# Kernel tuning notes

Hardware: AMD Instinct MI355X
Metric: run time of the kernel (lower is better)

The kernel has to match this reference:

```python
import jax, jax.numpy as jnp
import numpy as np

B, T, I, H = 256, 2000, 23, 128


def setup_inputs() -> dict:
    key = jax.random.key(0)
    ks = jax.random.split(key, 5)
    s = 1.0 / np.sqrt(H)  # PyTorch GRU init bound
    return {
        "x": jax.random.normal(ks[0], (B, T, I), dtype=jnp.float32),
        "W_ih": jax.random.uniform(ks[1], (3 * H, I), jnp.float32, -s, s),
        "W_hh": jax.random.uniform(ks[2], (3 * H, H), jnp.float32, -s, s),
        "b_ih": jax.random.uniform(ks[3], (3 * H,), jnp.float32, -s, s),
        "b_hh": jax.random.uniform(ks[4], (3 * H,), jnp.float32, -s, s),
    }


def reference(x, W_ih, W_hh, b_ih, b_hh):
    """Single-layer unidirectional GRU (PyTorch gate order r,z,n),
    followed by mean over time. Dropout is identity (eval mode)."""
    Bb, Tt, _ = x.shape
    Hh = W_hh.shape[1]
    # Precompute input-side gate projections for all timesteps: [T, B, 3H]
    gx = jnp.einsum('bti,gi->tbg', x, W_ih) + b_ih

    def step(h, g):
        gh = h @ W_hh.T + b_hh                               # [B, 3H]
        r = jax.nn.sigmoid(g[:, :Hh] + gh[:, :Hh])
        z = jax.nn.sigmoid(g[:, Hh:2 * Hh] + gh[:, Hh:2 * Hh])
        n = jnp.tanh(g[:, 2 * Hh:] + r * gh[:, 2 * Hh:])
        h_new = (1.0 - z) * n + z * h
        return h_new, h_new

    h0 = jnp.zeros((Bb, Hh), dtype=x.dtype)
    _, hs = jax.lax.scan(step, h0, gx)                       # hs: [T, B, H]
    return jnp.mean(hs, axis=0)                              # [B, H]
```

## Files before the change

### kernel.cpp

```cpp
#include <hip/hip_runtime.h>


#define Bb 256
#define Tt 2000
#define Ii 23
#define Hh 128

typedef float v2f __attribute__((ext_vector_type(2)));
typedef float v4f __attribute__((ext_vector_type(4)));

template <int N> struct ic { static constexpr int v = N; };

template <int ctrl>
__device__ __forceinline__ float dpp_movf(float v) {
    int r = __builtin_amdgcn_update_dpp(0, __builtin_bit_cast(int, v),
                                        ctrl, 0xf, 0xf, true);
    return __builtin_bit_cast(float, r);
}
__device__ __forceinline__ float swz_xor4(float v) {
    int r = __builtin_amdgcn_ds_swizzle(__builtin_bit_cast(int, v), 0x101F);
    return __builtin_bit_cast(float, r);
}
__device__ __forceinline__ void pk_fma(v2f& a, v2f b, v2f c) {
    asm("v_pk_fma_f32 %0, %1, %2, %0" : "+v"(a) : "v"(b), "v"(c));
}
__device__ __forceinline__ v2f pk_mul(v2f b, v2f c) {
    v2f d;
    asm("v_pk_mul_f32 %0, %1, %2" : "=v"(d) : "v"(b), "v"(c));
    return d;
}
__device__ __forceinline__ float fexp2(float x) {
#if __has_builtin(__builtin_amdgcn_exp2f)
    return __builtin_amdgcn_exp2f(x);
#else
    return exp2f(x);
#endif
}
__device__ __forceinline__ void bar_lds() {
    asm volatile("s_waitcnt lgkmcnt(0)\n\ts_barrier" ::: "memory");
}

__device__ __forceinline__ float fold16x8(const float a[8]) {
    float b0 = a[0] + dpp_movf<0xB1>(a[4]);
    float b1 = a[1] + dpp_movf<0xB1>(a[5]);
    float b2 = a[2] + dpp_movf<0xB1>(a[6]);
    float b3 = a[3] + dpp_movf<0xB1>(a[7]);
    float c0 = b0 + dpp_movf<0x4E>(b2);
    float c1 = b1 + dpp_movf<0x4E>(b3);
    float d  = c0 + swz_xor4(c1);
    return d + dpp_movf<0x128>(d);
}
__device__ __forceinline__ float fold16x4(const float a[4]) {
    float b0 = a[0] + dpp_movf<0xB1>(a[0]);
    float b1 = a[1] + dpp_movf<0xB1>(a[1]);
    float b2 = a[2] + dpp_movf<0xB1>(a[2]);
    float b3 = a[3] + dpp_movf<0xB1>(a[3]);
    float c0 = b0 + dpp_movf<0x4E>(b2);
    float c1 = b1 + dpp_movf<0x4E>(b3);
    float d  = c0 + swz_xor4(c1);
    return d + dpp_movf<0x128>(d);
}

__global__ __launch_bounds__(512, 2)
void gru_fused(const float* __restrict__ x,
               const float* __restrict__ W_ih,
               const float* __restrict__ W_hh,
               const float* __restrict__ b_ih,
               const float* __restrict__ b_hh,
               float* __restrict__ out)
{
    const int b   = blockIdx.x;
    const int tid = threadIdx.x;
    const int wid = tid >> 6;
    const int l   = tid & 63;
    const int kt  = l & 15;
    const int kb  = kt * 8;
    const int p   = ((kt & 1) << 2) | (kt & 2) | ((kt >> 2) & 1);
    const int p2  = (kt & 2) | ((kt >> 2) & 1);
    const int jbase = wid * 16 + ((l >> 4) << 2);

    __shared__ __align__(16) float h_db[2][16][12];

    const float L2E = 1.4426950408889634f;
    const float K2  = 2.0f * L2E;

    v2f wrz2[8][4];
    #pragma unroll
    for (int i = 0; i < 8; ++i) {
        const int u = i ^ p;
        const int g = (u >> 2) * Hh + jbase + (u & 3);
        const v2f* wp = reinterpret_cast<const v2f*>(W_hh + (size_t)g * Hh + kb);
        #pragma unroll
        for (int kk = 0; kk < 4; ++kk) {
            v2f w = wp[kk];
            w[0] *= L2E; w[1] *= L2E;
            wrz2[i][kk] = w;
        }
    }
    v2f wn2[4][4];
    #pragma unroll
    for (int q = 0; q < 4; ++q) {
        const int g = 2 * Hh + jbase + (q ^ p2);
        const v2f* wp = reinterpret_cast<const v2f*>(W_hh + (size_t)g * Hh + kb);
        #pragma unroll
        for (int kk = 0; kk < 4; ++kk) {
            v2f w = wp[kk];
            w[0] *= K2; w[1] *= K2;
            wn2[q][kk] = w;
        }
    }

    const int xi0  = (kt < 7) ? kt * 2 : 7 + kt;
    const int xoff = (kt < 7) ? 1 : 0;
    v2f wx2[8];
    #pragma unroll
    for (int i = 0; i < 8; ++i) {
        const int u = i ^ p;
        const int g = (u >> 2) * Hh + jbase + (u & 3);
        wx2[i][0] = W_ih[(size_t)g * Ii + xi0] * L2E;
        wx2[i][1] = xoff ? W_ih[(size_t)g * Ii + xi0 + 1] * L2E : 0.0f;
    }
    v2f wxn2[4];
    #pragma unroll
    for (int q = 0; q < 4; ++q) {
        const int g = 2 * Hh + jbase + (q ^ p2);
        wxn2[q][0] = W_ih[(size_t)g * Ii + xi0] * K2;
        wxn2[q][1] = xoff ? W_ih[(size_t)g * Ii + xi0 + 1] * K2 : 0.0f;
    }

    const int gp = (p >> 2) * Hh + jbase + (p & 3);
    const float brz_l = (b_ih[gp] + b_hh[gp]) * L2E;
    const int jn = jbase + p2;
    const float bhn_l = b_hh[2 * Hh + jn] * K2;
    const float bxn_l = b_ih[2 * Hh + jn] * K2;

    const float* xrow = x + (size_t)b * Tt * Ii;

    if (tid < Hh) h_db[0][tid >> 3][tid & 7] = 0.0f;
    float x0a = xrow[xi0],      x0b = xrow[xi0 + xoff];
    float x1a = xrow[Ii + xi0], x1b = xrow[Ii + xi0 + xoff];
    int xob = 2 * Ii + xi0;
    float h_reg = 0.0f, acc_mean = 0.0f;
    const bool writer = ((kt & 9) == 0);
    const int  jw = jbase + p;
    bar_lds();

    auto body = [&](auto CUR, int s) {
        constexpr int cur = decltype(CUR)::v;
        const int step = s + cur;

        const v4f hA = *reinterpret_cast<const v4f*>(&h_db[cur][kt][0]);
        const v4f hB = *reinterpret_cast<const v4f*>(&h_db[cur][kt][4]);
        v2f hp[4];
        hp[0] = __builtin_shufflevector(hA, hA, 0, 1);
        hp[1] = __builtin_shufflevector(hA, hA, 2, 3);
        hp[2] = __builtin_shufflevector(hB, hB, 0, 1);
        hp[3] = __builtin_shufflevector(hB, hB, 2, 3);

        v2f acc[8], accn[4];
        #pragma unroll
        for (int i = 0; i < 8; ++i) acc[i] = pk_mul(wrz2[i][0], hp[0]);
        #pragma unroll
        for (int q = 0; q < 4; ++q) accn[q] = pk_mul(wn2[q][0], hp[0]);
        #pragma unroll
        for (int kk = 1; kk < 4; ++kk) {
            #pragma unroll
            for (int i = 0; i < 8; ++i) pk_fma(acc[i], wrz2[i][kk], hp[kk]);
            #pragma unroll
            for (int q = 0; q < 4; ++q) pk_fma(accn[q], wn2[q][kk], hp[kk]);
        }

        v2f xpv;
        if constexpr (cur == 0) { xpv[0] = x0a; xpv[1] = x0b; }
        else                    { xpv[0] = x1a; xpv[1] = x1b; }
        #pragma unroll
        for (int i = 0; i < 8; ++i) pk_fma(acc[i], wx2[i], xpv);
        float arz[8];
        #pragma unroll
        for (int i = 0; i < 8; ++i) arz[i] = acc[i][0] + acc[i][1];
        float an[4], axn[4];
        #pragma unroll
        for (int q = 0; q < 4; ++q) {
            an[q] = accn[q][0] + accn[q][1];
            v2f tq = pk_mul(wxn2[q], xpv);
            axn[q] = tq[0] + tq[1];
        }

        if constexpr (cur == 0) { x0a = xrow[xob]; x0b = xrow[xob + xoff]; }
        else                    { x1a = xrow[xob]; x1b = xrow[xob + xoff]; }
        if (step + 3 < Tt) xob += Ii;

        const float rz_tot = fold16x8(arz) + brz_l;
        const float ghn = fold16x4(an) + bhn_l;
        const float gxn = fold16x4(axn) + bxn_l;

        const float zin = dpp_movf<0xB1>(rz_tot);
        const float r  = __builtin_amdgcn_rcpf(1.0f + fexp2(-rz_tot));
        const float z  = __builtin_amdgcn_rcpf(1.0f + fexp2(-zin));
        const float npre = fmaf(r, ghn, gxn);
        const float tt2  = __builtin_amdgcn_rcpf(1.0f + fexp2(-npre));
        const float nn   = fmaf(2.0f, tt2, -1.0f);
        const float h_new = fmaf(z, h_reg - nn, nn);
        h_reg = h_new;
        if (writer) {
            acc_mean += h_new;
            h_db[cur ^ 1][jw >> 3][jw & 7] = h_new;
        }
        bar_lds();
    };

    for (int s = 0; s < Tt; s += 2) {
        body(ic<0>{}, s);
        body(ic<1>{}, s);
    }

    if (writer) out[(size_t)b * Hh + jw] = acc_mean * (1.0f / Tt);
}

extern "C" void kernel_launch(void* const* d_in, const int* in_sizes, int n_in,
                              void* d_out, int out_size, void* d_ws, size_t ws_size,
                              hipStream_t stream) {
    const float* x    = (const float*)d_in[0];
    const float* W_ih = (const float*)d_in[1];
    const float* W_hh = (const float*)d_in[2];
    const float* b_ih = (const float*)d_in[3];
    const float* b_hh = (const float*)d_in[4];
    float* out = (float*)d_out;

    gru_fused<<<Bb, 512, 0, stream>>>(x, W_ih, W_hh, b_ih, b_hh, out);
}
```

Before: 1.275 ms.

## Repartition GRU recurrence: 4 lanes per hidden unit with 32-wide K slices

Changes the per-step work split so that each hidden unit j is computed by 4 adjacent lanes, each holding 32 K-elements of the r, z and n weight rows, replacing the 16-lane split with permuted gate assignment. The cross-lane reduction shrinks to two DPP adds per gate and the ds_swizzle step is gone, which shortens the serial critical path of each timestep. In exchange every lane now evaluates all three gates, so the transcendental work is duplicated across the 4 lanes. The h broadcast layout in LDS changes to 4 rows of 36 floats, and each lane now reads eight 16-byte vectors per step.

```diff
diff --git a/kernel.cpp b/kernel.cpp
--- a/kernel.cpp
+++ b/kernel.cpp
@@ -15,10 +15,6 @@
 __device__ __forceinline__ float dpp_movf(float v) {
     int r = __builtin_amdgcn_update_dpp(0, __builtin_bit_cast(int, v),
                                         ctrl, 0xf, 0xf, true);
-    return __builtin_bit_cast(float, r);
-}
-__device__ __forceinline__ float swz_xor4(float v) {
-    int r = __builtin_amdgcn_ds_swizzle(__builtin_bit_cast(int, v), 0x101F);
     return __builtin_bit_cast(float, r);
 }
 __device__ __forceinline__ void pk_fma(v2f& a, v2f b, v2f c) {
@@ -36,29 +32,15 @@
     return exp2f(x);
 #endif
 }
+__device__ __forceinline__ v2f pinv(v2f v) { asm("" : "+v"(v)); return v; }
+__device__ __forceinline__ float pinf(float v) { asm("" : "+v"(v)); return v; }
 __device__ __forceinline__ void bar_lds() {
     asm volatile("s_waitcnt lgkmcnt(0)\n\ts_barrier" ::: "memory");
 }
-
-__device__ __forceinline__ float fold16x8(const float a[8]) {
-    float b0 = a[0] + dpp_movf<0xB1>(a[4]);
-    float b1 = a[1] + dpp_movf<0xB1>(a[5]);
-    float b2 = a[2] + dpp_movf<0xB1>(a[6]);
-    float b3 = a[3] + dpp_movf<0xB1>(a[7]);
-    float c0 = b0 + dpp_movf<0x4E>(b2);
-    float c1 = b1 + dpp_movf<0x4E>(b3);
-    float d  = c0 + swz_xor4(c1);
-    return d + dpp_movf<0x128>(d);
-}
-__device__ __forceinline__ float fold16x4(const float a[4]) {
-    float b0 = a[0] + dpp_movf<0xB1>(a[0]);
-    float b1 = a[1] + dpp_movf<0xB1>(a[1]);
-    float b2 = a[2] + dpp_movf<0xB1>(a[2]);
-    float b3 = a[3] + dpp_movf<0xB1>(a[3]);
-    float c0 = b0 + dpp_movf<0x4E>(b2);
-    float c1 = b1 + dpp_movf<0x4E>(b3);
-    float d  = c0 + swz_xor4(c1);
-    return d + dpp_movf<0x128>(d);
+__device__ __forceinline__ float qfold(float c) {
+    c += dpp_movf<0xB1>(c);
+    c += dpp_movf<0x4E>(c);
+    return c;
 }
 
 __global__ __launch_bounds__(512, 2)
@@ -73,139 +55,130 @@
     const int tid = threadIdx.x;
     const int wid = tid >> 6;
     const int l   = tid & 63;
-    const int kt  = l & 15;
-    const int kb  = kt * 8;
-    const int p   = ((kt & 1) << 2) | (kt & 2) | ((kt >> 2) & 1);
-    const int p2  = (kt & 2) | ((kt >> 2) & 1);
-    const int jbase = wid * 16 + ((l >> 4) << 2);
-
-    __shared__ __align__(16) float h_db[2][16][12];
+    const int jj  = l >> 2;
+    const int kt  = l & 3;
+    const int j   = wid * 16 + jj;
+    const int kb  = kt * 32;
+
+    __shared__ __align__(16) float h_db[2][4][36];
 
     const float L2E = 1.4426950408889634f;
     const float K2  = 2.0f * L2E;
 
-    v2f wrz2[8][4];
-    #pragma unroll
-    for (int i = 0; i < 8; ++i) {
-        const int u = i ^ p;
-        const int g = (u >> 2) * Hh + jbase + (u & 3);
-        const v2f* wp = reinterpret_cast<const v2f*>(W_hh + (size_t)g * Hh + kb);
-        #pragma unroll
-        for (int kk = 0; kk < 4; ++kk) {
-            v2f w = wp[kk];
-            w[0] *= L2E; w[1] *= L2E;
-            wrz2[i][kk] = w;
-        }
-    }
-    v2f wn2[4][4];
-    #pragma unroll
-    for (int q = 0; q < 4; ++q) {
-        const int g = 2 * Hh + jbase + (q ^ p2);
-        const v2f* wp = reinterpret_cast<const v2f*>(W_hh + (size_t)g * Hh + kb);
-        #pragma unroll
-        for (int kk = 0; kk < 4; ++kk) {
-            v2f w = wp[kk];
-            w[0] *= K2; w[1] *= K2;
-            wn2[q][kk] = w;
-        }
-    }
-
-    const int xi0  = (kt < 7) ? kt * 2 : 7 + kt;
-    const int xoff = (kt < 7) ? 1 : 0;
-    v2f wx2[8];
-    #pragma unroll
-    for (int i = 0; i < 8; ++i) {
-        const int u = i ^ p;
-        const int g = (u >> 2) * Hh + jbase + (u & 3);
-        wx2[i][0] = W_ih[(size_t)g * Ii + xi0] * L2E;
-        wx2[i][1] = xoff ? W_ih[(size_t)g * Ii + xi0 + 1] * L2E : 0.0f;
-    }
-    v2f wxn2[4];
-    #pragma unroll
-    for (int q = 0; q < 4; ++q) {
-        const int g = 2 * Hh + jbase + (q ^ p2);
-        wxn2[q][0] = W_ih[(size_t)g * Ii + xi0] * K2;
-        wxn2[q][1] = xoff ? W_ih[(size_t)g * Ii + xi0 + 1] * K2 : 0.0f;
-    }
-
-    const int gp = (p >> 2) * Hh + jbase + (p & 3);
-    const float brz_l = (b_ih[gp] + b_hh[gp]) * L2E;
-    const int jn = jbase + p2;
-    const float bhn_l = b_hh[2 * Hh + jn] * K2;
-    const float bxn_l = b_ih[2 * Hh + jn] * K2;
-
-    const float* xrow = x + (size_t)b * Tt * Ii;
-
-    if (tid < Hh) h_db[0][tid >> 3][tid & 7] = 0.0f;
-    float x0a = xrow[xi0],      x0b = xrow[xi0 + xoff];
-    float x1a = xrow[Ii + xi0], x1b = xrow[Ii + xi0 + xoff];
-    int xob = 2 * Ii + xi0;
-    float h_reg = 0.0f, acc_mean = 0.0f;
-    const bool writer = ((kt & 9) == 0);
-    const int  jw = jbase + p;
+    v2f wr[16], wz[16], wn[16];
+    {
+        const float* Wr = W_hh + (size_t)j * Hh + kb;
+        const float* Wz = W_hh + (size_t)(Hh + j) * Hh + kb;
+        const float* Wn = W_hh + (size_t)(2 * Hh + j) * Hh + kb;
+        #pragma unroll
+        for (int kk = 0; kk < 16; ++kk) {
+            v2f a = *reinterpret_cast<const v2f*>(Wr + 2 * kk);
+            a[0] *= L2E; a[1] *= L2E; wr[kk] = pinv(a);
+            v2f c = *reinterpret_cast<const v2f*>(Wz + 2 * kk);
+            c[0] *= L2E; c[1] *= L2E; wz[kk] = pinv(c);
+            v2f d = *reinterpret_cast<const v2f*>(Wn + 2 * kk);
+            d[0] *= K2;  d[1] *= K2;  wn[kk] = pinv(d);
+        }
+    }
+
+    const int xi0 = (kt < 3) ? kt * 6 : 18;
+    const int xo2 = (kt < 3) ? 4 : 3;
+    v2f wxr[3], wxz[3], wxn[3];
+    {
+        const float* Xr = W_ih + (size_t)j * Ii;
+        const float* Xz = W_ih + (size_t)(Hh + j) * Ii;
+        const float* Xn = W_ih + (size_t)(2 * Hh + j) * Ii;
+        #pragma unroll
+        for (int m = 0; m < 3; ++m) {
+            const int e0 = xi0 + ((m < 2) ? 2 * m : xo2);
+            const float klo = (kt == 3 && m == 2) ? 0.0f : 1.0f;
+            v2f a; a[0] = Xr[e0] * L2E * klo; a[1] = Xr[e0 + 1] * L2E;
+            wxr[m] = pinv(a);
+            v2f c; c[0] = Xz[e0] * L2E * klo; c[1] = Xz[e0 + 1] * L2E;
+            wxz[m] = pinv(c);
+            v2f d; d[0] = Xn[e0] * K2 * klo;  d[1] = Xn[e0 + 1] * K2;
+            wxn[m] = pinv(d);
+        }
+    }
+
+    const float br  = pinf((b_ih[j] + b_hh[j]) * L2E);
+    const float bz  = pinf((b_ih[Hh + j] + b_hh[Hh + j]) * L2E);
+    const float bnh = pinf(b_hh[2 * Hh + j] * K2);
+    const float bnx = pinf(b_ih[2 * Hh + j] * K2);
+
+    const float* xrow = x + (size_t)b * Tt * Ii + xi0;
+
+    if (tid < Hh) h_db[0][tid >> 5][tid & 31] = 0.0f;
+    float xA[6], xB[6];
+    {
+        #pragma unroll
+        for (int m = 0; m < 4; ++m) { xA[m] = xrow[m]; xB[m] = xrow[Ii + m]; }
+        xA[4] = xrow[xo2];     xA[5] = xrow[xo2 + 1];
+        xB[4] = xrow[Ii + xo2]; xB[5] = xrow[Ii + xo2 + 1];
+    }
+    int xob = 2 * Ii;
+    float h_prev = 0.0f, acc_mean = 0.0f;
     bar_lds();
 
     auto body = [&](auto CUR, int s) {
         constexpr int cur = decltype(CUR)::v;
         const int step = s + cur;
 
-        const v4f hA = *reinterpret_cast<const v4f*>(&h_db[cur][kt][0]);
-        const v4f hB = *reinterpret_cast<const v4f*>(&h_db[cur][kt][4]);
-        v2f hp[4];
-        hp[0] = __builtin_shufflevector(hA, hA, 0, 1);
-        hp[1] = __builtin_shufflevector(hA, hA, 2, 3);
-        hp[2] = __builtin_shufflevector(hB, hB, 0, 1);
-        hp[3] = __builtin_shufflevector(hB, hB, 2, 3);
-
-        v2f acc[8], accn[4];
-        #pragma unroll
-        for (int i = 0; i < 8; ++i) acc[i] = pk_mul(wrz2[i][0], hp[0]);
-        #pragma unroll
-        for (int q = 0; q < 4; ++q) accn[q] = pk_mul(wn2[q][0], hp[0]);
-        #pragma unroll
-        for (int kk = 1; kk < 4; ++kk) {
+        v2f xp0, xp1, xp2;
+        if constexpr (cur == 0) {
+            xp0[0]=xA[0]; xp0[1]=xA[1]; xp1[0]=xA[2]; xp1[1]=xA[3];
+            xp2[0]=xA[4]; xp2[1]=xA[5];
+        } else {
+            xp0[0]=xB[0]; xp0[1]=xB[1]; xp1[0]=xB[2]; xp1[1]=xB[3];
+            xp2[0]=xB[4]; xp2[1]=xB[5];
+        }
+        v2f ar = pk_mul(wxr[0], xp0);
+        pk_fma(ar, wxr[1], xp1); pk_fma(ar, wxr[2], xp2);
+        v2f az = pk_mul(wxz[0], xp0);
+        pk_fma(az, wxz[1], xp1); pk_fma(az, wxz[2], xp2);
+        v2f ax = pk_mul(wxn[0], xp0);
+        pk_fma(ax, wxn[1], xp1); pk_fma(ax, wxn[2], xp2);
+
+        v2f ah;
+        #pragma unroll
+        for (int c = 0; c < 8; ++c) {
+            const v4f hc = *reinterpret_cast<const v4f*>(&h_db[cur][kt][4 * c]);
+            const v2f hpA = __builtin_shufflevector(hc, hc, 0, 1);
+            const v2f hpB = __builtin_shufflevector(hc, hc, 2, 3);
+            pk_fma(ar, wr[2 * c], hpA); pk_fma(ar, wr[2 * c + 1], hpB);
+            pk_fma(az, wz[2 * c], hpA); pk_fma(az, wz[2 * c + 1], hpB);
+            if (c == 0) {
+                ah = pk_mul(wn[0], hpA); pk_fma(ah, wn[1], hpB);
+            } else {
+                pk_fma(ah, wn[2 * c], hpA); pk_fma(ah, wn[2 * c + 1], hpB);
+            }
+        }
+
+        if constexpr (cur == 0) {
             #pragma unroll
-            for (int i = 0; i < 8; ++i) pk_fma(acc[i], wrz2[i][kk], hp[kk]);
+            for (int m = 0; m < 4; ++m) xA[m] = xrow[xob + m];
+            xA[4] = xrow[xob + xo2]; xA[5] = xrow[xob + xo2 + 1];
+        } else {
             #pragma unroll
-            for (int q = 0; q < 4; ++q) pk_fma(accn[q], wn2[q][kk], hp[kk]);
-        }
-
-        v2f xpv;
-        if constexpr (cur == 0) { xpv[0] = x0a; xpv[1] = x0b; }
-        else                    { xpv[0] = x1a; xpv[1] = x1b; }
-        #pragma unroll
-        for (int i = 0; i < 8; ++i) pk_fma(acc[i], wx2[i], xpv);
-        float arz[8];
-        #pragma unroll
-        for (int i = 0; i < 8; ++i) arz[i] = acc[i][0] + acc[i][1];
-        float an[4], axn[4];
-        #pragma unroll
-        for (int q = 0; q < 4; ++q) {
-            an[q] = accn[q][0] + accn[q][1];
-            v2f tq = pk_mul(wxn2[q], xpv);
-            axn[q] = tq[0] + tq[1];
-        }
-
-        if constexpr (cur == 0) { x0a = xrow[xob]; x0b = xrow[xob + xoff]; }
-        else                    { x1a = xrow[xob]; x1b = xrow[xob + xoff]; }
+            for (int m = 0; m < 4; ++m) xB[m] = xrow[xob + m];
+            xB[4] = xrow[xob + xo2]; xB[5] = xrow[xob + xo2 + 1];
+        }
         if (step + 3 < Tt) xob += Ii;
 
-        const float rz_tot = fold16x8(arz) + brz_l;
-        const float ghn = fold16x4(an) + bhn_l;
-        const float gxn = fold16x4(axn) + bxn_l;
-
-        const float zin = dpp_movf<0xB1>(rz_tot);
-        const float r  = __builtin_amdgcn_rcpf(1.0f + fexp2(-rz_tot));
-        const float z  = __builtin_amdgcn_rcpf(1.0f + fexp2(-zin));
+        const float r_s = qfold(ar[0] + ar[1]) + br;
+        const float z_s = qfold(az[0] + az[1]) + bz;
+        const float ghn = qfold(ah[0] + ah[1]) + bnh;
+        const float gxn = qfold(ax[0] + ax[1]) + bnx;
+
+        const float r  = __builtin_amdgcn_rcpf(1.0f + fexp2(-r_s));
+        const float z  = __builtin_amdgcn_rcpf(1.0f + fexp2(-z_s));
         const float npre = fmaf(r, ghn, gxn);
         const float tt2  = __builtin_amdgcn_rcpf(1.0f + fexp2(-npre));
         const float nn   = fmaf(2.0f, tt2, -1.0f);
-        const float h_new = fmaf(z, h_reg - nn, nn);
-        h_reg = h_new;
-        if (writer) {
-            acc_mean += h_new;
-            h_db[cur ^ 1][jw >> 3][jw & 7] = h_new;
-        }
+        const float h_new = fmaf(z, h_prev - nn, nn);
+        h_prev = h_new;
+        acc_mean += h_new;
+        if (kt == 0) h_db[cur ^ 1][j >> 5][j & 31] = h_new;
         bar_lds();
     };
 
@@ -214,7 +187,7 @@
         body(ic<1>{}, s);
     }
 
-    if (writer) out[(size_t)b * Hh + jw] = acc_mean * (1.0f / Tt);
+    if (kt == 0) out[(size_t)b * Hh + j] = acc_mean * (1.0f / Tt);
 }
 
 extern "C" void kernel_launch(void* const* d_in, const int* in_sizes, int n_in,
```

New measurement: 1.020 ms. 20.0% less time.
